# Performance work log

Measured on AMD Instinct MI355X. Metric: run time of the kernel, lower is better.

## Reference

```python
import jax, jax.numpy as jnp
import numpy as np

B, T, D = 2, 2048, 1024
H = 16
DH = D // H
SCALE = DH ** -0.5


def setup_inputs() -> dict:
    key = jax.random.key(0)
    ks = jax.random.split(key, 9)
    s = D ** -0.5
    return {
        "x": jax.random.normal(ks[0], (B, T, D), dtype=jnp.float32),
        "Wq": jax.random.normal(ks[1], (D, D), dtype=jnp.float32) * s,
        "bq": jax.random.normal(ks[2], (D,), dtype=jnp.float32) * 0.01,
        "Wk": jax.random.normal(ks[3], (D, D), dtype=jnp.float32) * s,
        "bk": jax.random.normal(ks[4], (D,), dtype=jnp.float32) * 0.01,
        "Wv": jax.random.normal(ks[5], (D, D), dtype=jnp.float32) * s,
        "bv": jax.random.normal(ks[6], (D,), dtype=jnp.float32) * 0.01,
        "Wo": jax.random.normal(ks[7], (D, D), dtype=jnp.float32) * s,
        "bo": jax.random.normal(ks[8], (D,), dtype=jnp.float32) * 0.01,
    }


def reference(x, Wq, bq, Wk, bk, Wv, bv, Wo, bo):
    # projections; torch Linear: y = x @ W.T + b. Here W is stored as (in, out).
    q = (x @ Wq + bq).reshape(B, T, H, DH).transpose(0, 2, 1, 3)  # (B,H,T,DH)
    k = (x @ Wk + bk).reshape(B, T, H, DH).transpose(0, 2, 1, 3)
    v = (x @ Wv + bv).reshape(B, T, H, DH).transpose(0, 2, 1, 3)
    scores = jnp.einsum("bhqd,bhkd->bhqk", q, k) * SCALE  # (B,H,T,T)
    causal = jnp.tril(jnp.ones((T, T), dtype=bool))
    scores = jnp.where(causal, scores, -jnp.inf)
    probs = jax.nn.softmax(scores, axis=-1)
    out = jnp.einsum("bhqk,bhkd->bhqd", probs, v)  # (B,H,T,DH)
    out = out.transpose(0, 2, 1, 3).reshape(B, T, D)
    out = out @ Wo + bo
    return out, (k, v)
```

## Files before the change

kernel.cpp:

```cpp
#include <hip/hip_runtime.h>

typedef float  f32x4  __attribute__((ext_vector_type(4)));
typedef float  f32x16 __attribute__((ext_vector_type(16)));
typedef __bf16 bf16x8 __attribute__((ext_vector_type(8)));
typedef short  s16x8  __attribute__((ext_vector_type(8)));
typedef short  s16x4  __attribute__((ext_vector_type(4)));
typedef unsigned int u32x4 __attribute__((ext_vector_type(4)));

static __device__ __forceinline__ unsigned short f2bf(float f) {
  return __builtin_bit_cast(unsigned short, (__bf16)f);
}
static __device__ __forceinline__ bf16x8 bc8(s16x8 v) {
  return __builtin_bit_cast(bf16x8, v);
}
static __device__ __forceinline__ f32x16 mfma32(bf16x8 a, bf16x8 b, f32x16 c) {
  return __builtin_amdgcn_mfma_f32_32x32x16_bf16(a, b, c, 0, 0, 0);
}
static __device__ __forceinline__ f32x4 mfma16(bf16x8 a, bf16x8 b, f32x4 c) {
  return __builtin_amdgcn_mfma_f32_16x16x32_bf16(a, b, c, 0, 0, 0);
}
static __device__ __forceinline__ unsigned pack2(float a, float b) {
  return ((unsigned)f2bf(b) << 16) | f2bf(a);
}

static __device__ __forceinline__ void gl2lds16(const unsigned short* g, unsigned short* l) {
  __builtin_amdgcn_global_load_lds(
      (const __attribute__((address_space(1))) unsigned int*)g,
      (__attribute__((address_space(3))) unsigned int*)l, 16, 0, 0);
}

#define GSYNC(NSTR)                                          \
  do {                                                       \
    __builtin_amdgcn_sched_barrier(0);                       \
    asm volatile("s_waitcnt vmcnt(" NSTR ")" ::: "memory");  \
    __builtin_amdgcn_s_barrier();                            \
    __builtin_amdgcn_sched_barrier(0);                       \
  } while (0)

__global__ void prep_k(const float* __restrict__ x, unsigned short* __restrict__ xb,
                       const float* __restrict__ W0, const float* __restrict__ W1,
                       const float* __restrict__ W2, const float* __restrict__ W3,
                       unsigned short* __restrict__ wtb) {
  __shared__ unsigned short tl[64][72];
  const int bid = blockIdx.x;
  const int t = threadIdx.x;
  if (bid < 2048) {
    int i = (bid * 256 + t) * 8;
    float4 a = *(const float4*)(x + i);
    float4 b = *(const float4*)(x + i + 4);
    s16x8 o;
    o[0] = (short)f2bf(a.x); o[1] = (short)f2bf(a.y);
    o[2] = (short)f2bf(a.z); o[3] = (short)f2bf(a.w);
    o[4] = (short)f2bf(b.x); o[5] = (short)f2bf(b.y);
    o[6] = (short)f2bf(b.z); o[7] = (short)f2bf(b.w);
    *(s16x8*)(xb + i) = o;
    return;
  }
  const int rid = bid - 2048;
  const int z = rid >> 8, rem = rid & 255;
  const float* W = z == 0 ? W0 : z == 1 ? W1 : z == 2 ? W2 : W3;
  unsigned short* out = wtb + (size_t)z * 1048576;
  const int nt = (rem & 15) * 64, kt = (rem >> 4) * 64;
  const int row = t >> 2, seg = t & 3;
  const float* src = W + (kt + row) * 1024 + nt + seg * 16;
#pragma unroll
  for (int q = 0; q < 4; ++q) {
    float4 v = *(const float4*)(src + q * 4);
    tl[seg * 16 + q * 4 + 0][row] = f2bf(v.x);
    tl[seg * 16 + q * 4 + 1][row] = f2bf(v.y);
    tl[seg * 16 + q * 4 + 2][row] = f2bf(v.z);
    tl[seg * 16 + q * 4 + 3][row] = f2bf(v.w);
  }
  __syncthreads();
  unsigned short* dst = out + (nt + row) * 1024 + kt + seg * 16;
  *(s16x8*)dst       = *(const s16x8*)&tl[row][seg * 16];
  *(s16x8*)(dst + 8) = *(const s16x8*)&tl[row][seg * 16 + 8];
}

static __device__ __forceinline__ int trans_ix(int m, int n) {
  int b = m >> 11, tt = m & 2047, h = n >> 6, dh = n & 63;
  return ((b << 4) + h) * 131072 + tt * 64 + dh;
}

__global__ __launch_bounds__(512, 4) void gemm_qkv_k(const unsigned short* __restrict__ A,
                                                     const unsigned short* __restrict__ BT,
                                                     const float* __restrict__ b0,
                                                     const float* __restrict__ b1,
                                                     const float* __restrict__ b2,
                                                     float* __restrict__ outF,
                                                     unsigned short* __restrict__ oq,
                                                     unsigned short* __restrict__ ok,
                                                     unsigned short* __restrict__ ov) {
  extern __shared__ unsigned short lds[];
  const int t = threadIdx.x;
  const int lane = t & 63, ln = lane & 15, g = lane >> 4;
  const int w = t >> 6, wm = w >> 2, wn = w & 3;
  const unsigned wgid = blockIdx.x;
  const unsigned swz = (wgid & 7) * 64 + (wgid >> 3);
  const int by = swz & 31, bx = swz >> 5;
  const int bm0 = by * 128, bn0 = bx * 192;

  const int ar = t >> 2;
  const unsigned short* aBase = A + (size_t)(bm0 + ar) * 1024 + (((t & 3) ^ ((ar >> 1) & 3)) * 8);
  const int br = t >> 3;
  const int bcol = (t & 7) ^ (br & 7);
  const unsigned short* bBase = BT + (size_t)(bn0 + br) * 1024 + bcol * 8;

  auto issueA = [&](int buf, int H, int kt) {
    gl2lds16(aBase + kt + H * 32, &lds[buf * 20480 + H * 4096 + t * 8]);
  };
  auto issueB = [&](int buf, int j, int kt) {
    gl2lds16(bBase + (size_t)j * 65536 + kt, &lds[buf * 20480 + 8192 + j * 4096 + t * 8]);
  };
  auto ldA = [&](int buf, int H, int mf) -> bf16x8 {
    const int row = wm * 64 + mf * 16 + ln;
    const int sp = g ^ ((row >> 1) & 3);
    return bc8(*(const s16x8*)&lds[buf * 20480 + H * 4096 + row * 32 + sp * 8]);
  };
  auto ldB = [&](int buf, int H, int nf) -> bf16x8 {
    const int row = wn * 48 + nf * 16 + ln;
    const int sp = (H * 4 + g) ^ (row & 7);
    return bc8(*(const s16x8*)&lds[buf * 20480 + 8192 + row * 64 + sp * 8]);
  };

  f32x4 acc[4][3] = {};
  issueA(0, 0, 0);
  issueB(0, 0, 0);
  issueB(0, 1, 0);
  issueB(0, 2, 0);
  issueA(0, 1, 0);

  for (int ti = 0; ti < 16; ++ti) {
    const int buf = ti & 1, nb = buf ^ 1;
    const bool hn = ti < 15;
    const int kn = (ti + 1) * 64;

    GSYNC("1");
    if (hn) { issueA(nb, 0, kn); issueB(nb, 0, kn); issueB(nb, 1, kn); }
    {
      bf16x8 afr[4], bfr[3];
#pragma unroll
      for (int mf = 0; mf < 4; ++mf) afr[mf] = ldA(buf, 0, mf);
#pragma unroll
      for (int nf = 0; nf < 3; ++nf) bfr[nf] = ldB(buf, 0, nf);
      __builtin_amdgcn_s_setprio(1);
#pragma unroll
      for (int mf = 0; mf < 4; ++mf)
#pragma unroll
        for (int nf = 0; nf < 3; ++nf) acc[mf][nf] = mfma16(afr[mf], bfr[nf], acc[mf][nf]);
      __builtin_amdgcn_s_setprio(0);
    }
    if (hn) GSYNC("3"); else GSYNC("0");
    if (hn) { issueB(nb, 2, kn); issueA(nb, 1, kn); }
    {
      bf16x8 afr[4], bfr[3];
#pragma unroll
      for (int mf = 0; mf < 4; ++mf) afr[mf] = ldA(buf, 1, mf);
#pragma unroll
      for (int nf = 0; nf < 3; ++nf) bfr[nf] = ldB(buf, 1, nf);
      __builtin_amdgcn_s_setprio(1);
#pragma unroll
      for (int mf = 0; mf < 4; ++mf)
#pragma unroll
        for (int nf = 0; nf < 3; ++nf) acc[mf][nf] = mfma16(afr[mf], bfr[nf], acc[mf][nf]);
      __builtin_amdgcn_s_setprio(0);
    }
  }

#pragma unroll
  for (int nf = 0; nf < 3; ++nf) {
    const int n = bn0 + wn * 48 + nf * 16 + ln;
    const int n1 = n & 1023;
    const float* bp = n < 1024 ? b0 : (n < 2048 ? b1 : b2);
    const float bias = bp[n1];
#pragma unroll
    for (int mf = 0; mf < 4; ++mf)
#pragma unroll
      for (int r = 0; r < 4; ++r) {
        const int m = bm0 + wm * 64 + mf * 16 + g * 4 + r;
        const float v = acc[mf][nf][r] + bias;
        const int ix = trans_ix(m, n1);
        if (n < 1024) {
          oq[ix] = f2bf(v * 0.18033688f);
        } else if (n < 2048) {
          ok[ix] = f2bf(v);
          outF[4194304 + ix] = v;
        } else {
          ov[ix] = f2bf(v);
          outF[8388608 + ix] = v;
        }
      }
  }
}

__global__ __launch_bounds__(512, 4) void gemm_o_k(const unsigned short* __restrict__ A,
                                                   const unsigned short* __restrict__ BT,
                                                   const float* __restrict__ b0,
                                                   float* __restrict__ outF) {
  extern __shared__ unsigned short lds[];
  const int t = threadIdx.x;
  const int lane = t & 63, ln = lane & 15, g = lane >> 4;
  const int w = t >> 6, wm = w >> 2, wn = w & 3;
  const unsigned wgid = blockIdx.x;
  const unsigned swz = (wgid & 7) * 64 + (wgid >> 3);
  const int bx = swz & 7, by = swz >> 3;
  const int bm0 = by * 64, bn0 = bx * 128;

  const int row = t >> 3;
  const int scol = (t & 7) ^ (row & 7);
  const unsigned short* aSrc = A + (size_t)(bm0 + row) * 1024 + scol * 8;
  const unsigned short* bSrc0 = BT + (size_t)(bn0 + row) * 1024 + scol * 8;
  const unsigned short* bSrc1 = BT + (size_t)(bn0 + 64 + row) * 1024 + scol * 8;

  auto issue3 = [&](int buf, int ti) {
    const int kt = ti * 64;
    gl2lds16(aSrc + kt, &lds[buf * 12288 + t * 8]);
    gl2lds16(bSrc0 + kt, &lds[buf * 12288 + 4096 + t * 8]);
    gl2lds16(bSrc1 + kt, &lds[buf * 12288 + 8192 + t * 8]);
  };
  auto ldA = [&](int buf, int H, int mf) -> bf16x8 {
    const int r = wm * 32 + mf * 16 + ln;
    const int sp = (H * 4 + g) ^ (r & 7);
    return bc8(*(const s16x8*)&lds[buf * 12288 + r * 64 + sp * 8]);
  };
  auto ldB = [&](int buf, int H, int nf) -> bf16x8 {
    const int r = wn * 32 + nf * 16 + ln;
    const int j = r >> 6, rl = r & 63;
    const int sp = (H * 4 + g) ^ (rl & 7);
    return bc8(*(const s16x8*)&lds[buf * 12288 + 4096 + j * 4096 + rl * 64 + sp * 8]);
  };

  f32x4 acc[2][2] = {};
  issue3(0, 0);
  issue3(1, 1);

  for (int i = 0; i < 16; ++i) {
    const int buf = i & 1;
    if (i < 15) GSYNC("3"); else GSYNC("0");
    bf16x8 a0[2], a1[2], bq0[2], bq1[2];
#pragma unroll
    for (int mf = 0; mf < 2; ++mf) { a0[mf] = ldA(buf, 0, mf); a1[mf] = ldA(buf, 1, mf); }
#pragma unroll
    for (int nf = 0; nf < 2; ++nf) { bq0[nf] = ldB(buf, 0, nf); bq1[nf] = ldB(buf, 1, nf); }
    asm volatile("s_waitcnt lgkmcnt(0)" ::: "memory");
    __builtin_amdgcn_sched_barrier(0);
    __builtin_amdgcn_s_barrier();
    __builtin_amdgcn_sched_barrier(0);
    if (i + 2 < 16) issue3(buf, i + 2);
    __builtin_amdgcn_s_setprio(1);
#pragma unroll
    for (int mf = 0; mf < 2; ++mf)
#pragma unroll
      for (int nf = 0; nf < 2; ++nf) {
        acc[mf][nf] = mfma16(a0[mf], bq0[nf], acc[mf][nf]);
        acc[mf][nf] = mfma16(a1[mf], bq1[nf], acc[mf][nf]);
      }
    __builtin_amdgcn_s_setprio(0);
  }

#pragma unroll
  for (int nf = 0; nf < 2; ++nf) {
    const int n = bn0 + wn * 32 + nf * 16 + ln;
    const float bias = b0[n];
#pragma unroll
    for (int mf = 0; mf < 2; ++mf)
#pragma unroll
      for (int r = 0; r < 4; ++r) {
        const int m = bm0 + wm * 32 + mf * 16 + g * 4 + r;
        outF[(size_t)m * 1024 + n] = acc[mf][nf][r] + bias;
      }
  }
}

__global__ __launch_bounds__(512) void attn_k(const unsigned short* __restrict__ qb,
                                              const unsigned short* __restrict__ kb,
                                              const unsigned short* __restrict__ vb,
                                              unsigned short* __restrict__ ob) {
  __shared__ s16x8 kS[2][2][512];
  __shared__ s16x8 vS[2][2][512];
  const int t = threadIdx.x;
  const int lane = t & 63, l31 = lane & 31, h5 = lane >> 5;
  const int w = t >> 6, grp = w >> 2, qw = w & 3;
  const unsigned wg = blockIdx.x;
  const int x = wg & 7, r_ = wg >> 3;
  const int bh = x + 8 * (r_ >> 3);
  const int p = r_ & 7;
  const int b = bh >> 4, h = bh & 15;
  const unsigned short* Qp = qb + (size_t)bh * 131072;
  const unsigned short* Kp = kb + (size_t)bh * 131072;
  const unsigned short* Vp = vb + (size_t)bh * 131072;

  const int tp = t & 255;
  const int krow = tp >> 2, kseg = tp & 3;
  const int dhb = tp >> 4, kvb_ = tp & 15;

  float* mg0 = (float*)&kS[0][0][0];
  float* mg1 = (float*)&vS[0][0][0];
  float* ml = mg0 + 17 * 256;
  const int slot = qw * 64 + lane;

  for (int half = 0; half < 2; ++half) {
    const int qblk = half == 0 ? p : 15 - p;
    const int q0 = qblk * 128;
    const int NT = qblk + 1;
    const int tbase = grp * NT;
    const int qg = q0 + qw * 32 + l31;

    bf16x8 qf[4];
#pragma unroll
    for (int m = 0; m < 4; ++m)
      qf[m] = bc8(*(const s16x8*)(Qp + (size_t)qg * 64 + 16 * m + 8 * h5));

    f32x16 o0 = {}, o1 = {};
    float lrow = 0.f;

    __syncthreads();
    {
      const int kv0 = tbase * 64;
      const s16x8* ks = (const s16x8*)(Kp + (kv0 + krow) * 64 + kseg * 16);
      s16x8 k0 = ks[0], k1 = ks[1];
      kS[grp][0][krow * 8 + ((2 * kseg) ^ (krow & 7))]     = k0;
      kS[grp][0][krow * 8 + ((2 * kseg + 1) ^ (krow & 7))] = k1;
      s16x4 vj[4];
#pragma unroll
      for (int jj = 0; jj < 4; ++jj)
        vj[jj] = *(const s16x4*)(Vp + (kv0 + kvb_ * 4 + jj) * 64 + dhb * 4);
      short* vbase = (short*)&vS[grp][0][0];
#pragma unroll
      for (int dd = 0; dd < 4; ++dd) {
        const int d = (dd + dhb) & 3;
        const int row = dhb * 4 + d;
        s16x4 wv;
        wv[0] = vj[0][d]; wv[1] = vj[1][d]; wv[2] = vj[2][d]; wv[3] = vj[3][d];
        *(s16x4*)(vbase + row * 64 + ((kvb_ >> 1) ^ (row & 7)) * 8 + (kvb_ & 1) * 4) = wv;
      }
    }
    __syncthreads();

    for (int i = 0; i < NT; ++i) {
      const int buf = i & 1;
      const bool pre = (i + 1) < NT;
      const int kv0 = (tbase + i) * 64;
      s16x8 pk0, pk1;
      s16x4 pvj[4];
      if (pre) {
        const int kv1 = kv0 + 64;
        const s16x8* ks = (const s16x8*)(Kp + (kv1 + krow) * 64 + kseg * 16);
        pk0 = ks[0];
        pk1 = ks[1];
#pragma unroll
        for (int jj = 0; jj < 4; ++jj)
          pvj[jj] = *(const s16x4*)(Vp + (kv1 + kvb_ * 4 + jj) * 64 + dhb * 4);
      }

      const bool active = (kv0 <= q0 + qw * 32 + 31);
      if (active) {
        f32x16 s0 = {}, s1 = {};
        const s16x8* kb_ = &kS[grp][buf][0];
#pragma unroll
        for (int m = 0; m < 4; ++m) {
          const int sl = 2 * m + h5;
          bf16x8 a0 = bc8(kb_[l31 * 8 + (sl ^ (l31 & 7))]);
          bf16x8 a1 = bc8(kb_[(l31 + 32) * 8 + (sl ^ (l31 & 7))]);
          s0 = mfma32(a0, qf[m], s0);
          s1 = mfma32(a1, qf[m], s1);
        }
        if (kv0 + 63 > q0 + qw * 32) {
#pragma unroll
          for (int r = 0; r < 16; ++r) {
            const int kvr = kv0 + (r & 3) + 8 * (r >> 2) + 4 * h5;
            if (kvr > qg) s0[r] = -1e30f;
            if (kvr + 32 > qg) s1[r] = -1e30f;
          }
        }
        float ps = 0.f;
#pragma unroll
        for (int r = 0; r < 16; ++r) {
          s0[r] = exp2f(s0[r]);
          s1[r] = exp2f(s1[r]);
          ps += s0[r] + s1[r];
        }
        ps += __shfl_xor(ps, 32);
        lrow += ps;

        unsigned og[2][4][2];
#pragma unroll
        for (int gg = 0; gg < 4; ++gg) {
          og[0][gg][0] = pack2(s0[4 * gg], s0[4 * gg + 1]);
          og[0][gg][1] = pack2(s0[4 * gg + 2], s0[4 * gg + 3]);
          og[1][gg][0] = pack2(s1[4 * gg], s1[4 * gg + 1]);
          og[1][gg][1] = pack2(s1[4 * gg + 2], s1[4 * gg + 3]);
        }
        bf16x8 pf[4];
#pragma unroll
        for (int mp = 0; mp < 4; ++mp) {
          const int tau = mp >> 1, lc = mp & 1;
          unsigned a0 = og[tau][2 * lc][0], bq0 = og[tau][2 * lc + 1][0];
          unsigned a1 = og[tau][2 * lc][1], bq1 = og[tau][2 * lc + 1][1];
          asm volatile("v_permlane32_swap_b32 %0, %1" : "+v"(a0), "+v"(bq0));
          asm volatile("v_permlane32_swap_b32 %0, %1" : "+v"(a1), "+v"(bq1));
          u32x4 fw; fw[0] = a0; fw[1] = a1; fw[2] = bq0; fw[3] = bq1;
          pf[mp] = __builtin_bit_cast(bf16x8, fw);
        }
        const s16x8* vb2 = &vS[grp][buf][0];
#pragma unroll
        for (int mp = 0; mp < 4; ++mp) {
          const int sl = 2 * mp + h5;
          bf16x8 va0 = bc8(vb2[l31 * 8 + (sl ^ (l31 & 7))]);
          bf16x8 va1 = bc8(vb2[(l31 + 32) * 8 + (sl ^ (l31 & 7))]);
          o0 = mfma32(va0, pf[mp], o0);
          o1 = mfma32(va1, pf[mp], o1);
        }
      }

      if (pre) {
        const int ob_ = buf ^ 1;
        kS[grp][ob_][krow * 8 + ((2 * kseg) ^ (krow & 7))]     = pk0;
        kS[grp][ob_][krow * 8 + ((2 * kseg + 1) ^ (krow & 7))] = pk1;
        short* vbase = (short*)&vS[grp][ob_][0];
#pragma unroll
        for (int dd = 0; dd < 4; ++dd) {
          const int d = (dd + dhb) & 3;
          const int row = dhb * 4 + d;
          s16x4 wv;
          wv[0] = pvj[0][d]; wv[1] = pvj[1][d]; wv[2] = pvj[2][d]; wv[3] = pvj[3][d];
          *(s16x4*)(vbase + row * 64 + ((kvb_ >> 1) ^ (row & 7)) * 8 + (kvb_ & 1) * 4) = wv;
        }
        __syncthreads();
      }
    }

    __syncthreads();
    if (grp == 1) {
#pragma unroll
      for (int r = 0; r < 16; ++r) mg0[slot * 17 + r] = o0[r];
#pragma unroll
      for (int r = 0; r < 16; ++r) mg1[slot * 17 + r] = o1[r];
      ml[slot] = lrow;
    }
    __syncthreads();
    if (grp == 0) {
      const float inv = 1.0f / (lrow + ml[slot]);
      unsigned short* orow = ob + (size_t)(b * 2048 + qg) * 1024 + h * 64;
#pragma unroll
      for (int rq = 0; rq < 4; ++rq) {
        s16x4 ov0, ov1;
#pragma unroll
        for (int e = 0; e < 4; ++e) {
          ov0[e] = (short)f2bf((o0[4 * rq + e] + mg0[slot * 17 + 4 * rq + e]) * inv);
          ov1[e] = (short)f2bf((o1[4 * rq + e] + mg1[slot * 17 + 4 * rq + e]) * inv);
        }
        *(s16x4*)(orow + 8 * rq + 4 * h5)      = ov0;
        *(s16x4*)(orow + 32 + 8 * rq + 4 * h5) = ov1;
      }
    }
  }
}

extern "C" void kernel_launch(void* const* d_in, const int* in_sizes, int n_in,
                              void* d_out, int out_size, void* d_ws, size_t ws_size,
                              hipStream_t stream) {
  (void)in_sizes; (void)n_in; (void)out_size; (void)ws_size;
  const float* x  = (const float*)d_in[0];
  const float* Wq = (const float*)d_in[1];
  const float* bq = (const float*)d_in[2];
  const float* Wk = (const float*)d_in[3];
  const float* bk = (const float*)d_in[4];
  const float* Wv = (const float*)d_in[5];
  const float* bv = (const float*)d_in[6];
  const float* Wo = (const float*)d_in[7];
  const float* bo = (const float*)d_in[8];
  float* out = (float*)d_out;

  unsigned short* ws  = (unsigned short*)d_ws;
  unsigned short* xb  = ws;
  unsigned short* wtb = ws + 4194304;
  unsigned short* qbuf = ws + 8388608;
  unsigned short* kbuf = qbuf + 4194304;
  unsigned short* vbuf = kbuf + 4194304;
  unsigned short* ab   = vbuf + 4194304;

  prep_k<<<3072, 256, 0, stream>>>(x, xb, Wq, Wk, Wv, Wo, wtb);
  gemm_qkv_k<<<512, 512, 81920, stream>>>(xb, wtb, bq, bk, bv, out, qbuf, kbuf, vbuf);
  attn_k<<<256, 512, 0, stream>>>(qbuf, kbuf, vbuf, ab);
  gemm_o_k<<<512, 512, 49152, stream>>>(ab, wtb + 3145728, bo, out);
}
```

Before: 110.1 us.

## Pre-transpose V in QKV epilogue and triple-buffer attention K/V via direct-to-LDS loads

After: 95.74 us. -13.0%, faster.

```diff
diff --git a/kernel.cpp b/kernel.cpp
--- a/kernel.cpp
+++ b/kernel.cpp
@@ -18,9 +18,6 @@
 }
 static __device__ __forceinline__ f32x4 mfma16(bf16x8 a, bf16x8 b, f32x4 c) {
   return __builtin_amdgcn_mfma_f32_16x16x32_bf16(a, b, c, 0, 0, 0);
-}
-static __device__ __forceinline__ unsigned pack2(float a, float b) {
-  return ((unsigned)f2bf(b) << 16) | f2bf(a);
 }
 
 static __device__ __forceinline__ void gl2lds16(const unsigned short* g, unsigned short* l) {
@@ -90,7 +87,7 @@
                                                      float* __restrict__ outF,
                                                      unsigned short* __restrict__ oq,
                                                      unsigned short* __restrict__ ok,
-                                                     unsigned short* __restrict__ ov) {
+                                                     unsigned short* __restrict__ ovT) {
   extern __shared__ unsigned short lds[];
   const int t = threadIdx.x;
   const int lane = t & 63, ln = lane & 15, g = lane >> 4;
@@ -173,23 +170,41 @@
     const int n1 = n & 1023;
     const float* bp = n < 1024 ? b0 : (n < 2048 ? b1 : b2);
     const float bias = bp[n1];
-#pragma unroll
-    for (int mf = 0; mf < 4; ++mf)
-#pragma unroll
-      for (int r = 0; r < 4; ++r) {
-        const int m = bm0 + wm * 64 + mf * 16 + g * 4 + r;
-        const float v = acc[mf][nf][r] + bias;
-        const int ix = trans_ix(m, n1);
-        if (n < 1024) {
-          oq[ix] = f2bf(v * 0.18033688f);
-        } else if (n < 2048) {
+    if (n < 1024) {
+#pragma unroll
+      for (int mf = 0; mf < 4; ++mf)
+#pragma unroll
+        for (int r = 0; r < 4; ++r) {
+          const int m = bm0 + wm * 64 + mf * 16 + g * 4 + r;
+          oq[trans_ix(m, n1)] = f2bf((acc[mf][nf][r] + bias) * 0.18033688f);
+        }
+    } else if (n < 2048) {
+#pragma unroll
+      for (int mf = 0; mf < 4; ++mf)
+#pragma unroll
+        for (int r = 0; r < 4; ++r) {
+          const int m = bm0 + wm * 64 + mf * 16 + g * 4 + r;
+          const float v = acc[mf][nf][r] + bias;
+          const int ix = trans_ix(m, n1);
           ok[ix] = f2bf(v);
           outF[4194304 + ix] = v;
-        } else {
-          ov[ix] = f2bf(v);
-          outF[8388608 + ix] = v;
-        }
+        }
+    } else {
+      const int dh = n1 & 63, hh = n1 >> 6;
+#pragma unroll
+      for (int mf = 0; mf < 4; ++mf) {
+        const int m0 = bm0 + wm * 64 + mf * 16 + g * 4;
+        const int bb = m0 >> 11, tt = m0 & 2047;
+        s16x4 pv;
+#pragma unroll
+        for (int r = 0; r < 4; ++r) {
+          const float v = acc[mf][nf][r] + bias;
+          outF[8388608 + trans_ix(m0 + r, n1)] = v;
+          pv[r] = (short)f2bf(v);
+        }
+        *(s16x4*)(ovT + (size_t)((bb << 4) + hh) * 131072 + (size_t)dh * 2048 + tt) = pv;
       }
+    }
   }
 }
 
@@ -274,10 +289,9 @@
 
 __global__ __launch_bounds__(512) void attn_k(const unsigned short* __restrict__ qb,
                                               const unsigned short* __restrict__ kb,
-                                              const unsigned short* __restrict__ vb,
+                                              const unsigned short* __restrict__ vbT,
                                               unsigned short* __restrict__ ob) {
-  __shared__ s16x8 kS[2][2][512];
-  __shared__ s16x8 vS[2][2][512];
+  extern __shared__ s16x8 kvS[];
   const int t = threadIdx.x;
   const int lane = t & 63, l31 = lane & 31, h5 = lane >> 5;
   const int w = t >> 6, grp = w >> 2, qw = w & 3;
@@ -288,15 +302,23 @@
   const int b = bh >> 4, h = bh & 15;
   const unsigned short* Qp = qb + (size_t)bh * 131072;
   const unsigned short* Kp = kb + (size_t)bh * 131072;
-  const unsigned short* Vp = vb + (size_t)bh * 131072;
-
-  const int tp = t & 255;
-  const int krow = tp >> 2, kseg = tp & 3;
-  const int dhb = tp >> 4, kvb_ = tp & 15;
-
-  float* mg0 = (float*)&kS[0][0][0];
-  float* mg1 = (float*)&vS[0][0][0];
-  float* ml = mg0 + 17 * 256;
+  const unsigned short* Vp = vbT + (size_t)bh * 131072;
+
+  const int e0 = qw * 64 + lane;
+  const int kr0 = e0 >> 3;
+  const int kcol = (e0 & 7) ^ (kr0 & 7);
+  const unsigned short* kSrc = Kp + (size_t)kr0 * 64 + kcol * 8;
+  const unsigned short* vSrc = Vp + (size_t)kr0 * 2048 + kcol * 8;
+  s16x8* gB = &kvS[grp * 3072];
+
+  s16x8 onesv;
+#pragma unroll
+  for (int z = 0; z < 8; ++z) onesv[z] = (short)0x3F80;
+  const bf16x8 onesf = bc8(onesv);
+
+  float* mg0 = (float*)&kvS[0];
+  float* mg1 = mg0 + 4352;
+  float* ml  = mg0 + 8704;
   const int slot = qw * 64 + lane;
 
   for (int half = 0; half < 2; ++half) {
@@ -306,57 +328,39 @@
     const int tbase = grp * NT;
     const int qg = q0 + qw * 32 + l31;
 
+    __syncthreads();
+
     bf16x8 qf[4];
 #pragma unroll
     for (int m = 0; m < 4; ++m)
       qf[m] = bc8(*(const s16x8*)(Qp + (size_t)qg * 64 + 16 * m + 8 * h5));
 
-    f32x16 o0 = {}, o1 = {};
-    float lrow = 0.f;
-
-    __syncthreads();
-    {
-      const int kv0 = tbase * 64;
-      const s16x8* ks = (const s16x8*)(Kp + (kv0 + krow) * 64 + kseg * 16);
-      s16x8 k0 = ks[0], k1 = ks[1];
-      kS[grp][0][krow * 8 + ((2 * kseg) ^ (krow & 7))]     = k0;
-      kS[grp][0][krow * 8 + ((2 * kseg + 1) ^ (krow & 7))] = k1;
-      s16x4 vj[4];
-#pragma unroll
-      for (int jj = 0; jj < 4; ++jj)
-        vj[jj] = *(const s16x4*)(Vp + (kv0 + kvb_ * 4 + jj) * 64 + dhb * 4);
-      short* vbase = (short*)&vS[grp][0][0];
-#pragma unroll
-      for (int dd = 0; dd < 4; ++dd) {
-        const int d = (dd + dhb) & 3;
-        const int row = dhb * 4 + d;
-        s16x4 wv;
-        wv[0] = vj[0][d]; wv[1] = vj[1][d]; wv[2] = vj[2][d]; wv[3] = vj[3][d];
-        *(s16x4*)(vbase + row * 64 + ((kvb_ >> 1) ^ (row & 7)) * 8 + (kvb_ & 1) * 4) = wv;
-      }
-    }
-    __syncthreads();
-
+    auto issue = [&](int ti, int buf) {
+      const int kv0 = (tbase + ti) * 64;
+      unsigned short* kd = (unsigned short*)&gB[buf * 1024];
+      unsigned short* vd = (unsigned short*)&gB[buf * 1024 + 512];
+      const unsigned short* ks = kSrc + (size_t)kv0 * 64;
+      const unsigned short* vs = vSrc + kv0;
+      gl2lds16(ks,         kd + e0 * 8);
+      gl2lds16(ks + 2048,  kd + (e0 + 256) * 8);
+      gl2lds16(vs,         vd + e0 * 8);
+      gl2lds16(vs + 65536, vd + (e0 + 256) * 8);
+    };
+
+    issue(0, 0);
+    if (NT > 1) issue(1, 1);
+
+    f32x16 o0 = {}, o1 = {}, lsum = {};
+    int buf = 0;
     for (int i = 0; i < NT; ++i) {
-      const int buf = i & 1;
-      const bool pre = (i + 1) < NT;
+      if (i + 1 < NT) GSYNC("4"); else GSYNC("0");
+      if (i + 2 < NT) issue(i + 2, buf == 0 ? 2 : buf - 1);
       const int kv0 = (tbase + i) * 64;
-      s16x8 pk0, pk1;
-      s16x4 pvj[4];
-      if (pre) {
-        const int kv1 = kv0 + 64;
-        const s16x8* ks = (const s16x8*)(Kp + (kv1 + krow) * 64 + kseg * 16);
-        pk0 = ks[0];
-        pk1 = ks[1];
-#pragma unroll
-        for (int jj = 0; jj < 4; ++jj)
-          pvj[jj] = *(const s16x4*)(Vp + (kv1 + kvb_ * 4 + jj) * 64 + dhb * 4);
-      }
-
       const bool active = (kv0 <= q0 + qw * 32 + 31);
       if (active) {
+        const s16x8* kb_ = &gB[buf * 1024];
+        const s16x8* vb2 = &gB[buf * 1024 + 512];
         f32x16 s0 = {}, s1 = {};
-        const s16x8* kb_ = &kS[grp][buf][0];
 #pragma unroll
         for (int m = 0; m < 4; ++m) {
           const int sl = 2 * m + h5;
@@ -373,23 +377,18 @@
             if (kvr + 32 > qg) s1[r] = -1e30f;
           }
         }
-        float ps = 0.f;
 #pragma unroll
         for (int r = 0; r < 16; ++r) {
-          s0[r] = exp2f(s0[r]);
-          s1[r] = exp2f(s1[r]);
-          ps += s0[r] + s1[r];
-        }
-        ps += __shfl_xor(ps, 32);
-        lrow += ps;
-
+          s0[r] = __builtin_amdgcn_exp2f(s0[r]);
+          s1[r] = __builtin_amdgcn_exp2f(s1[r]);
+        }
         unsigned og[2][4][2];
 #pragma unroll
         for (int gg = 0; gg < 4; ++gg) {
-          og[0][gg][0] = pack2(s0[4 * gg], s0[4 * gg + 1]);
-          og[0][gg][1] = pack2(s0[4 * gg + 2], s0[4 * gg + 3]);
-          og[1][gg][0] = pack2(s1[4 * gg], s1[4 * gg + 1]);
-          og[1][gg][1] = pack2(s1[4 * gg + 2], s1[4 * gg + 3]);
+          asm("v_cvt_pk_bf16_f32 %0, %1, %2" : "=v"(og[0][gg][0]) : "v"(s0[4 * gg]),     "v"(s0[4 * gg + 1]));
+          asm("v_cvt_pk_bf16_f32 %0, %1, %2" : "=v"(og[0][gg][1]) : "v"(s0[4 * gg + 2]), "v"(s0[4 * gg + 3]));
+          asm("v_cvt_pk_bf16_f32 %0, %1, %2" : "=v"(og[1][gg][0]) : "v"(s1[4 * gg]),     "v"(s1[4 * gg + 1]));
+          asm("v_cvt_pk_bf16_f32 %0, %1, %2" : "=v"(og[1][gg][1]) : "v"(s1[4 * gg + 2]), "v"(s1[4 * gg + 3]));
         }
         bf16x8 pf[4];
 #pragma unroll
@@ -402,7 +401,6 @@
           u32x4 fw; fw[0] = a0; fw[1] = a1; fw[2] = bq0; fw[3] = bq1;
           pf[mp] = __builtin_bit_cast(bf16x8, fw);
         }
-        const s16x8* vb2 = &vS[grp][buf][0];
 #pragma unroll
         for (int mp = 0; mp < 4; ++mp) {
           const int sl = 2 * mp + h5;
@@ -410,24 +408,10 @@
           bf16x8 va1 = bc8(vb2[(l31 + 32) * 8 + (sl ^ (l31 & 7))]);
           o0 = mfma32(va0, pf[mp], o0);
           o1 = mfma32(va1, pf[mp], o1);
+          lsum = mfma32(onesf, pf[mp], lsum);
         }
       }
-
-      if (pre) {
-        const int ob_ = buf ^ 1;
-        kS[grp][ob_][krow * 8 + ((2 * kseg) ^ (krow & 7))]     = pk0;
-        kS[grp][ob_][krow * 8 + ((2 * kseg + 1) ^ (krow & 7))] = pk1;
-        short* vbase = (short*)&vS[grp][ob_][0];
-#pragma unroll
-        for (int dd = 0; dd < 4; ++dd) {
-          const int d = (dd + dhb) & 3;
-          const int row = dhb * 4 + d;
-          s16x4 wv;
-          wv[0] = pvj[0][d]; wv[1] = pvj[1][d]; wv[2] = pvj[2][d]; wv[3] = pvj[3][d];
-          *(s16x4*)(vbase + row * 64 + ((kvb_ >> 1) ^ (row & 7)) * 8 + (kvb_ & 1) * 4) = wv;
-        }
-        __syncthreads();
-      }
+      buf = (buf == 2) ? 0 : buf + 1;
     }
 
     __syncthreads();
@@ -436,11 +420,11 @@
       for (int r = 0; r < 16; ++r) mg0[slot * 17 + r] = o0[r];
 #pragma unroll
       for (int r = 0; r < 16; ++r) mg1[slot * 17 + r] = o1[r];
-      ml[slot] = lrow;
+      ml[slot] = lsum[0];
     }
     __syncthreads();
     if (grp == 0) {
-      const float inv = 1.0f / (lrow + ml[slot]);
+      const float inv = 1.0f / (lsum[0] + ml[slot]);
       unsigned short* orow = ob + (size_t)(b * 2048 + qg) * 1024 + h * 64;
 #pragma unroll
       for (int rq = 0; rq < 4; ++rq) {
@@ -482,6 +466,6 @@
 
   prep_k<<<3072, 256, 0, stream>>>(x, xb, Wq, Wk, Wv, Wo, wtb);
   gemm_qkv_k<<<512, 512, 81920, stream>>>(xb, wtb, bq, bk, bv, out, qbuf, kbuf, vbuf);
-  attn_k<<<256, 512, 0, stream>>>(qbuf, kbuf, vbuf, ab);
+  attn_k<<<256, 512, 98304, stream>>>(qbuf, kbuf, vbuf, ab);
   gemm_o_k<<<512, 512, 49152, stream>>>(ab, wtb + 3145728, bo, out);
 }
```
